# Optimization experiments

Measured on AMD Instinct MI355X. Metric: run time of the kernel, lower is better.

Reference implementation:

```python
import jax, jax.numpy as jnp
import numpy as np

B, S, H, NH = 2, 2048, 2048, 16
HD = H // NH  # head_dim = 128


def setup_inputs() -> dict:
    key = jax.random.key(0)
    ks = jax.random.split(key, 6)
    scale = 1.0 / np.sqrt(H)
    hidden_state = jax.random.normal(ks[0], (B, S, H), dtype=jnp.float32)
    # upper-triangular (strictly above diagonal) = 1 -> masked positions
    causal_mask = jnp.triu(jnp.ones((S, S), dtype=jnp.float32), k=1)[None, None]
    Wq = jax.random.normal(ks[1], (H, H), dtype=jnp.float32) * scale
    Wk = jax.random.normal(ks[2], (H, H), dtype=jnp.float32) * scale
    Wv = jax.random.normal(ks[3], (H, H), dtype=jnp.float32) * scale
    Wo = jax.random.normal(ks[4], (H, H), dtype=jnp.float32) * scale
    zeros = jnp.zeros((H,), dtype=jnp.float32)
    return {"hidden_state": hidden_state, "causal_mask": causal_mask,
            "Wq": Wq, "bq": zeros, "Wk": Wk, "bk": zeros,
            "Wv": Wv, "bv": zeros, "Wo": Wo, "bo": zeros}


def reference(hidden_state, causal_mask, Wq, bq, Wk, bk, Wv, bv, Wo, bo):
    b, s, h = hidden_state.shape
    q = (hidden_state @ Wq.T + bq).reshape(b, s, NH, HD).transpose(0, 2, 1, 3)  # [B,NH,S,HD]
    k = (hidden_state @ Wk.T + bk).reshape(b, s, NH, HD).transpose(0, 2, 1, 3)
    v = (hidden_state @ Wv.T + bv).reshape(b, s, NH, HD).transpose(0, 2, 1, 3)
    scores = jnp.einsum('bhqd,bhkd->bhqk', q, k) / jnp.sqrt(jnp.float32(HD))
    scores = scores + causal_mask * (-1e9)
    probs = jax.nn.softmax(scores, axis=-1)
    out = jnp.einsum('bhqk,bhkd->bhqd', probs, v)
    out = out.transpose(0, 2, 1, 3).reshape(b, s, h)
    return out @ Wo.T + bo
```

## Files before the change

kernel.cpp:

```cpp
#include <hip/hip_runtime.h>
#include <hip/hip_bf16.h>
#include <stdint.h>

#define B_   2
#define S_   2048
#define H_   2048
#define NH_  16
#define HD_  128
#define MTOT (B_*S_)

typedef __attribute__((ext_vector_type(8))) short bf16x8;
typedef __attribute__((ext_vector_type(4))) short bf16x4;
typedef __attribute__((ext_vector_type(4))) float f32x4;

__device__ __forceinline__ void gload_lds16(const void* g, void* l) {
    __builtin_amdgcn_global_load_lds(
        (const __attribute__((address_space(1))) void*)g,
        (__attribute__((address_space(3))) void*)l, 16, 0, 0);
}

__device__ __forceinline__ unsigned short f2bfu(float x) {
    __hip_bfloat16 h = __float2bfloat16(x);
    return *reinterpret_cast<unsigned short*>(&h);
}
__device__ __forceinline__ int packbf(float a, float b) {
    return (int)f2bfu(a) | ((int)f2bfu(b) << 16);
}

#define BAR()  asm volatile("s_barrier" ::: "memory")
#define WLG0() asm volatile("s_waitcnt lgkmcnt(0)" ::: "memory")
#define WVM(n) asm volatile("s_waitcnt vmcnt(" #n ")" ::: "memory")

__global__ void castall(const float* __restrict__ hs,
                        const float* __restrict__ w0, const float* __restrict__ w1,
                        const float* __restrict__ w2, const float* __restrict__ w3,
                        __hip_bfloat16* __restrict__ xb,
                        __hip_bfloat16* __restrict__ o0, __hip_bfloat16* __restrict__ o1,
                        __hip_bfloat16* __restrict__ o2, __hip_bfloat16* __restrict__ o3)
{
    const size_t Q = 1048576;
    const float* in; __hip_bfloat16* out; size_t base = 0;
    switch (blockIdx.y) {
        case 0:  in = hs; out = xb; break;
        case 1:  in = hs; out = xb; base = Q; break;
        case 2:  in = w0; out = o0; break;
        case 3:  in = w1; out = o1; break;
        case 4:  in = w2; out = o2; break;
        default: in = w3; out = o3; break;
    }
    size_t i = base + (size_t)blockIdx.x * 256 + threadIdx.x;
    float4 v = *(const float4*)(in + i * 4);
    uint2 o;
    o.x = (unsigned)packbf(v.x, v.y);
    o.y = (unsigned)packbf(v.z, v.w);
    *(uint2*)((char*)out + i * 8) = o;
}

template<int EPI>
__device__ __forceinline__ void gemm256x128_body(const __hip_bfloat16* __restrict__ Xp,
                                                 const __hip_bfloat16* __restrict__ Wp,
                                                 const float* __restrict__ bias,
                                                 void* __restrict__ Cout,
                                                 int bm, int bn, char* smem)
{
    const int tid  = threadIdx.x;
    const int wave = tid >> 6, lane = tid & 63;
    const int quad = lane >> 4, l16 = lane & 15;
    const int wr = wave >> 2, wc = wave & 3;

    const int ro = l16 * 64;
    const int co = (((l16 & 8) ? ((quad * 8) ^ 16) : (quad * 8)) << 1);

    int r0, c0, r1, c1;
    {
        int D = tid * 16;
        int rg = D >> 11, cg = (D >> 10) & 1;
        int rr = (D >> 6) & 15, c = (D & 63) >> 1;
        int cs = (rr & 8) ? (c ^ 16) : c;
        r0 = rg * 16 + rr;  c0 = cg * 32 + cs;
        D = 8192 + tid * 16;
        rg = D >> 11; cg = (D >> 10) & 1;
        rr = (D >> 6) & 15; c = (D & 63) >> 1;
        cs = (rr & 8) ? (c ^ 16) : c;
        r1 = rg * 16 + rr;  c1 = cg * 32 + cs;
    }

    char* const A0h = smem + wr * 16384;
    char* const A1h = smem + 32768 + wr * 16384;
    char* const B0h = smem + 65536 + (wc >> 1) * 8192;
    char* const B1h = smem + 81920 + (wc >> 1) * 8192;
    const int bsub = (wc & 1) * 2;

    auto STG = [&](char* ldsb, const __hip_bfloat16* g) {
        gload_lds16(g + (size_t)r0 * H_ + c0, ldsb + wave * 1024);
        gload_lds16(g + (size_t)r1 * H_ + c1, ldsb + 8192 + wave * 1024);
    };
    auto STG1 = [&](char* ldsb, const __hip_bfloat16* g) {
        gload_lds16(g + (size_t)r0 * H_ + c0, ldsb + wave * 1024);
    };
    auto SRCA = [&](const __hip_bfloat16* P, int t, int hf) {
        return P + (size_t)(hf * 128) * H_ + (size_t)t * 64;
    };
    auto SRCB = [&](const __hip_bfloat16* P, int t, int hf) {
        return P + (size_t)(hf * 64) * H_ + (size_t)t * 64;
    };

    f32x4 acc[8][2] = {};

    STG (smem,          SRCA(Xp, 0, 0));
    STG (smem + 16384,  SRCA(Xp, 0, 1));
    STG1(smem + 65536,        SRCB(Wp, 0, 0));
    STG1(smem + 65536 + 8192, SRCB(Wp, 0, 1));
    STG1(smem + 81920,        SRCB(Wp, 1, 0));
    STG1(smem + 81920 + 8192, SRCB(Wp, 1, 1));
    WVM(2);
    BAR();

    const int NIT = H_ / 128;
    bf16x8 bfr[2][2];
    for (int j = 0; j < NIT; ++j) {
        const bool more = (j < NIT - 1);
        const int t1 = 2 * j + 1;
#pragma unroll
        for (int ph = 0; ph < 8; ++ph) {
            const int p = ph & 3;
            char* aA = (ph < 4) ? A0h : A1h;
            char* aB = (ph < 4) ? B0h : B1h;

            if (p == 0) {
#pragma unroll
                for (int jj = 0; jj < 2; ++jj)
#pragma unroll
                    for (int kk = 0; kk < 2; ++kk)
                        bfr[jj][kk] = *(const bf16x8*)(aB + ((bsub + jj) * 2 + kk) * 1024 + ro + co);
            }
            bf16x8 af[2][2];
#pragma unroll
            for (int i2 = 0; i2 < 2; ++i2)
#pragma unroll
                for (int kk = 0; kk < 2; ++kk)
                    af[i2][kk] = *(const bf16x8*)(aA + ((2 * p + i2) * 2 + kk) * 1024 + ro + co);

            if (ph == 0) { STG(smem + 32768, SRCA(Xp, t1, 0));
                           STG(smem + 49152, SRCA(Xp, t1, 1)); }
            else if (ph == 1 && more) STG1(smem + 65536,        SRCB(Wp, t1 + 1, 0));
            else if (ph == 2 && more) STG1(smem + 65536 + 8192, SRCB(Wp, t1 + 1, 1));
            else if (ph == 4 && more) STG (smem,                SRCA(Xp, t1 + 1, 0));
            else if (ph == 5 && more) STG (smem + 16384,        SRCA(Xp, t1 + 1, 1));
            else if (ph == 6 && more) STG1(smem + 81920,        SRCB(Wp, t1 + 2, 0));
            else if (ph == 7 && more) STG1(smem + 81920 + 8192, SRCB(Wp, t1 + 2, 1));

            if (ph == 3) { if (more) { WVM(2); } else { WVM(0); } }
            if (ph == 7 && more) { WVM(2); }

            BAR();
            WLG0();
            __builtin_amdgcn_sched_barrier(0);
            __builtin_amdgcn_s_setprio(1);
#pragma unroll
            for (int kk = 0; kk < 2; ++kk)
#pragma unroll
                for (int i2 = 0; i2 < 2; ++i2)
#pragma unroll
                    for (int jj = 0; jj < 2; ++jj)
                        acc[2 * p + i2][jj] = __builtin_amdgcn_mfma_f32_16x16x32_bf16(
                            af[i2][kk], bfr[jj][kk], acc[2 * p + i2][jj], 0, 0, 0);
            __builtin_amdgcn_s_setprio(0);
            BAR();
        }
    }

    if (EPI == 2) {
        __hip_bfloat16* VTo = (__hip_bfloat16*)Cout;
#pragma unroll
        for (int i = 0; i < 8; ++i) {
            int tok = bm * 256 + wr * 128 + i * 16 + quad * 4;
            int b = tok >> 11, s = tok & (S_ - 1);
#pragma unroll
            for (int jj = 0; jj < 2; ++jj) {
                int col = bn * 128 + (wc >> 1) * 64 + (wc & 1) * 32 + jj * 16 + l16;
                int h = col >> 7, d = col & 127;
                float bv = bias[col];
                bf16x4 v;
#pragma unroll
                for (int r = 0; r < 4; ++r)
                    v[r] = (short)f2bfu(acc[i][jj][r] + bv);
                *(bf16x4*)(VTo + ((size_t)(b * 16 + h) * 128 + d) * S_ + s) = v;
            }
        }
    } else {
#pragma unroll
        for (int i = 0; i < 8; ++i) {
            int row = bm * 256 + wr * 128 + i * 16 + quad * 4;
#pragma unroll
            for (int jj = 0; jj < 2; ++jj) {
                int col = bn * 128 + (wc >> 1) * 64 + (wc & 1) * 32 + jj * 16 + l16;
                float bv = bias[col];
#pragma unroll
                for (int r = 0; r < 4; ++r) {
                    float v = acc[i][jj][r] + bv;
                    if (EPI == 1)
                        ((__hip_bfloat16*)Cout)[(size_t)(row + r) * H_ + col] = __float2bfloat16(v);
                    else
                        ((float*)Cout)[(size_t)(row + r) * H_ + col] = v;
                }
            }
        }
    }
}

__global__ __launch_bounds__(512, 2)
void gemm_qkv8(const __hip_bfloat16* __restrict__ X,
               const __hip_bfloat16* __restrict__ Wq, const __hip_bfloat16* __restrict__ Wk,
               const __hip_bfloat16* __restrict__ Wv,
               const float* __restrict__ bq, const float* __restrict__ bk,
               const float* __restrict__ bv,
               __hip_bfloat16* __restrict__ Qo, __hip_bfloat16* __restrict__ Ko,
               __hip_bfloat16* __restrict__ VTo)
{
    __shared__ __align__(16) char smem[98304];

    const int bid = blockIdx.x;
    const int swz = (bid & 7) * 96 + (bid >> 3);
    const int sel = swz >> 8;
    const int rem = swz & 255;
    const int bn  = rem & 15;
    const int bm  = rem >> 4;

    const __hip_bfloat16* W = (sel == 0) ? Wq : (sel == 1) ? Wk : Wv;
    const float* bias       = (sel == 0) ? bq : (sel == 1) ? bk : bv;

    const __hip_bfloat16* Xp = X + (size_t)(bm * 256) * H_;
    const __hip_bfloat16* Wp = W + (size_t)(bn * 128) * H_;

    if (sel == 2)
        gemm256x128_body<2>(Xp, Wp, bias, VTo, bm, bn, smem);
    else
        gemm256x128_body<1>(Xp, Wp, bias, (sel == 0) ? Qo : Ko, bm, bn, smem);
}

__global__ __launch_bounds__(512, 2)
void gemm_out8(const __hip_bfloat16* __restrict__ A, const __hip_bfloat16* __restrict__ W,
               const float* __restrict__ bias, float* __restrict__ C)
{
    __shared__ __align__(16) char smem[98304];
    const int bid = blockIdx.x;
    const int swz = (bid & 7) * 32 + (bid >> 3);
    const int bn  = swz & 15;
    const int bm  = swz >> 4;
    gemm256x128_body<0>(A + (size_t)(bm * 256) * H_, W + (size_t)(bn * 128) * H_,
                        bias, C, bm, bn, smem);
}

__global__ __launch_bounds__(256, 2)
void attn_kernel(const __hip_bfloat16* __restrict__ Q,
                 const __hip_bfloat16* __restrict__ K,
                 const __hip_bfloat16* __restrict__ VT,
                 __hip_bfloat16* __restrict__ O)
{
    __shared__ __align__(16) char Ks[2][16384];
    __shared__ __align__(16) char Vt[2][16384];

    const int tid  = threadIdx.x;
    const int wave = tid >> 6, lane = tid & 63;
    const int quad = lane >> 4, l16 = lane & 15;

    const int lid = blockIdx.x;
    const int xcd = lid & 7;
    const int q   = lid >> 3;
    const int grp = q >> 4;
    const int k15 = q & 15;
    const int bh  = (grp << 3) | xcd;
    const int u   = (grp < 2) ? (15 - k15) : k15;
    const int b   = bh >> 4, h = bh & 15;
    const int qbA = 2 * u, qbB = 2 * u + 1;

    const size_t headoff = (size_t)b * S_ * H_ + (size_t)h * HD_;
    const __hip_bfloat16* Qp  = Q + headoff;
    const __hip_bfloat16* Kp  = K + headoff;
    const __hip_bfloat16* Vtp = VT + (size_t)(b * 16 + h) * 128 * S_;

    const float scale  = 0.08838834764831843f;
    const float THRraw = 90.50966799187809f;
    const int A0 = (((quad & 1) * 2) * 16 + l16) * 4;
    const int A1 = A0 + 64;
    const bool hiq = (quad >= 2);

    const int qrow_local = wave * 16;
    const int qrowA = qbA * 64 + qrow_local;
    const int qrowB = qbB * 64 + qrow_local;

    bf16x8 qfA[4], qfB[4];
#pragma unroll
    for (int kd = 0; kd < 4; ++kd) {
        qfA[kd] = *(const bf16x8*)(Qp + (size_t)(qrowA + l16) * H_ + kd * 32 + quad * 8);
        qfB[kd] = *(const bf16x8*)(Qp + (size_t)(qrowB + l16) * H_ + kd * 32 + quad * 8);
    }

    f32x4 oaccA[8] = {}, oaccB[8] = {};
    float miA = -1e30f, liA = 0.0f;
    float miB = -1e30f, liB = 0.0f;

    auto sm_xform = [&](f32x4 (&sacc)[4], float& mi, float& li, f32x4 (&oacc)[8],
                        bool diag, bf16x8 (&pf)[2]) {
        float p[4][4];
        float tm = -1e30f;
#pragma unroll
        for (int cb = 0; cb < 4; ++cb)
#pragma unroll
            for (int r = 0; r < 4; ++r) {
                float s = sacc[cb][r];
                if (diag) {
                    int keyl = cb * 16 + quad * 4 + r;
                    if (keyl > qrow_local + l16) s = -1e30f;
                }
                p[cb][r] = s;
                tm = fmaxf(tm, s);
            }
        tm = fmaxf(tm, __shfl_xor(tm, 16));
        tm = fmaxf(tm, __shfl_xor(tm, 32));

        const bool noresc = __all(tm - mi <= THRraw);
        float mnew = noresc ? mi : fmaxf(mi, tm);
        float ms = mnew * scale;

        float sum = 0.0f;
#pragma unroll
        for (int cb = 0; cb < 4; ++cb)
#pragma unroll
            for (int r = 0; r < 4; ++r) {
                float e = __expf(__builtin_fmaf(p[cb][r], scale, -ms));
                p[cb][r] = e;
                sum += e;
            }
        sum += __shfl_xor(sum, 16);
        sum += __shfl_xor(sum, 32);

        if (noresc) {
            li = li + sum;
        } else {
            float alpha = __expf((mi - mnew) * scale);
            li = li * alpha + sum;
            float ar[4];
#pragma unroll
            for (int r = 0; r < 4; ++r)
                ar[r] = __shfl(alpha, quad * 4 + r);
#pragma unroll
            for (int db = 0; db < 8; ++db)
#pragma unroll
                for (int r = 0; r < 4; ++r)
                    oacc[db][r] *= ar[r];
        }
        mi = mnew;

        int Pp[4][2];
#pragma unroll
        for (int cb = 0; cb < 4; ++cb) {
            Pp[cb][0] = packbf(p[cb][0], p[cb][1]);
            Pp[cb][1] = packbf(p[cb][2], p[cb][3]);
        }
#pragma unroll
        for (int ks = 0; ks < 2; ++ks) {
            int c0 = 2 * ks, c1 = 2 * ks + 1;
            int d0 = __builtin_amdgcn_ds_bpermute(A0, Pp[c0][0]);
            int e0 = __builtin_amdgcn_ds_bpermute(A0, Pp[c1][0]);
            int d1 = __builtin_amdgcn_ds_bpermute(A0, Pp[c0][1]);
            int e1 = __builtin_amdgcn_ds_bpermute(A0, Pp[c1][1]);
            int d2 = __builtin_amdgcn_ds_bpermute(A1, Pp[c0][0]);
            int e2 = __builtin_amdgcn_ds_bpermute(A1, Pp[c1][0]);
            int d3 = __builtin_amdgcn_ds_bpermute(A1, Pp[c0][1]);
            int e3 = __builtin_amdgcn_ds_bpermute(A1, Pp[c1][1]);
            union { int i[4]; bf16x8 v; } w;
            w.i[0] = hiq ? e0 : d0;
            w.i[1] = hiq ? e1 : d1;
            w.i[2] = hiq ? e2 : d2;
            w.i[3] = hiq ? e3 : d3;
            pf[ks] = w.v;
        }
    };

#pragma unroll
    for (int t = 0; t < 4; ++t) {
        int c = wave * 256 + t * 64 + lane;
        int krow = c >> 4, kpos = c & 15;
        gload_lds16(Kp + (size_t)krow * H_ + (kpos ^ (krow & 7)) * 8,
                    &Ks[0][(wave * 256 + t * 64) * 16]);
        int vrow = c >> 3, vpos = c & 7;
        gload_lds16(Vtp + (size_t)vrow * S_ + (vpos ^ (vrow & 7)) * 8,
                    &Vt[0][(wave * 256 + t * 64) * 16]);
    }
    __syncthreads();

    for (int kb = 0; kb <= qbB; ++kb) {
        const int cur = kb & 1;
        const bool more   = (kb < qbB);
        const bool aliveA = (kb <= qbA);

        if (more) {
            const __hip_bfloat16* Kn = Kp + (size_t)(kb + 1) * 64 * H_;
            const int vcol = (kb + 1) * 64;
#pragma unroll
            for (int t = 0; t < 4; ++t) {
                int c = wave * 256 + t * 64 + lane;
                int krow = c >> 4, kpos = c & 15;
                gload_lds16(Kn + (size_t)krow * H_ + (kpos ^ (krow & 7)) * 8,
                            &Ks[cur ^ 1][(wave * 256 + t * 64) * 16]);
                int vrow = c >> 3, vpos = c & 7;
                gload_lds16(Vtp + (size_t)vrow * S_ + vcol + (vpos ^ (vrow & 7)) * 8,
                            &Vt[cur ^ 1][(wave * 256 + t * 64) * 16]);
            }
        }

        f32x4 saccA[4] = {}, saccB[4] = {};
#pragma unroll
        for (int cb = 0; cb < 4; ++cb) {
#pragma unroll
            for (int kd = 0; kd < 4; ++kd) {
                int row = cb * 16 + l16;
                int pos = (4 * kd + quad) ^ (l16 & 7);
                bf16x8 kf = *(const bf16x8*)&Ks[cur][row * 256 + pos * 16];
                saccA[cb] = __builtin_amdgcn_mfma_f32_16x16x32_bf16(kf, qfA[kd], saccA[cb], 0, 0, 0);
                saccB[cb] = __builtin_amdgcn_mfma_f32_16x16x32_bf16(kf, qfB[kd], saccB[cb], 0, 0, 0);
            }
        }

        bf16x8 pfA[2], pfB[2];
        if (aliveA) sm_xform(saccA, miA, liA, oaccA, kb == qbA, pfA);
        sm_xform(saccB, miB, liB, oaccB, kb == qbB, pfB);

        if (aliveA) {
#pragma unroll
            for (int ks = 0; ks < 2; ++ks)
#pragma unroll
                for (int db = 0; db < 8; ++db) {
                    int vrow = db * 16 + l16;
                    int vpos = (ks * 4 + quad) ^ (l16 & 7);
                    bf16x8 vf = *(const bf16x8*)&Vt[cur][vrow * 128 + vpos * 16];
                    oaccA[db] = __builtin_amdgcn_mfma_f32_16x16x32_bf16(pfA[ks], vf, oaccA[db], 0, 0, 0);
                    oaccB[db] = __builtin_amdgcn_mfma_f32_16x16x32_bf16(pfB[ks], vf, oaccB[db], 0, 0, 0);
                }
        } else {
#pragma unroll
            for (int ks = 0; ks < 2; ++ks)
#pragma unroll
                for (int db = 0; db < 8; ++db) {
                    int vrow = db * 16 + l16;
                    int vpos = (ks * 4 + quad) ^ (l16 & 7);
                    bf16x8 vf = *(const bf16x8*)&Vt[cur][vrow * 128 + vpos * 16];
                    oaccB[db] = __builtin_amdgcn_mfma_f32_16x16x32_bf16(pfB[ks], vf, oaccB[db], 0, 0, 0);
                }
        }

        __syncthreads();
    }

    {
        float lr[4];
#pragma unroll
        for (int r = 0; r < 4; ++r)
            lr[r] = __shfl(liA, quad * 4 + r);
#pragma unroll
        for (int db = 0; db < 8; ++db)
#pragma unroll
            for (int r = 0; r < 4; ++r) {
                float v = oaccA[db][r] / lr[r];
                size_t row = (size_t)b * S_ + qrowA + quad * 4 + r;
                O[row * H_ + h * HD_ + db * 16 + l16] = __float2bfloat16(v);
            }
    }
    {
        float lr[4];
#pragma unroll
        for (int r = 0; r < 4; ++r)
            lr[r] = __shfl(liB, quad * 4 + r);
#pragma unroll
        for (int db = 0; db < 8; ++db)
#pragma unroll
            for (int r = 0; r < 4; ++r) {
                float v = oaccB[db][r] / lr[r];
                size_t row = (size_t)b * S_ + qrowB + quad * 4 + r;
                O[row * H_ + h * HD_ + db * 16 + l16] = __float2bfloat16(v);
            }
    }
}

extern "C" void kernel_launch(void* const* d_in, const int* in_sizes, int n_in,
                              void* d_out, int out_size, void* d_ws, size_t ws_size,
                              hipStream_t stream)
{
    const float* hs = (const float*)d_in[0];
    const float* Wq = (const float*)d_in[2];
    const float* bq = (const float*)d_in[3];
    const float* Wk = (const float*)d_in[4];
    const float* bk = (const float*)d_in[5];
    const float* Wv = (const float*)d_in[6];
    const float* bv = (const float*)d_in[7];
    const float* Wo = (const float*)d_in[8];
    const float* bo = (const float*)d_in[9];

    const size_t szX = (size_t)MTOT * H_;
    const size_t szW = (size_t)H_ * H_;

    __hip_bfloat16* Xbf = (__hip_bfloat16*)d_ws;
    __hip_bfloat16* Wqb = Xbf + szX;
    __hip_bfloat16* Wkb = Wqb + szW;
    __hip_bfloat16* Wvb = Wkb + szW;
    __hip_bfloat16* Wob = Wvb + szW;
    __hip_bfloat16* Qb  = Wob + szW;
    __hip_bfloat16* Kb  = Qb + szX;
    __hip_bfloat16* VTb = Kb + szX;

    castall<<<dim3(4096, 6), 256, 0, stream>>>(hs, Wq, Wk, Wv, Wo, Xbf, Wqb, Wkb, Wvb, Wob);

    gemm_qkv8<<<dim3(768), 512, 0, stream>>>(Xbf, Wqb, Wkb, Wvb, bq, bk, bv, Qb, Kb, VTb);

    attn_kernel<<<dim3(512), 256, 0, stream>>>(Qb, Kb, VTb, Xbf);

    gemm_out8<<<dim3(256), 512, 0, stream>>>(Xbf, Wob, bo, (float*)d_out);
}
```

Baseline: 371.6 us.

## Fuse Q and K projections into one block sharing the X tile

Adds a QK body in which each block computes both the Q and K output tiles for the same X rows. The X tile is loaded once from LDS and fed to two sets of MFMAs. This cuts X global loads and the block count for the QKV projection from 768 to 512 blocks, with 256 of them doing double work. In exchange the kernel needs 128KB of LDS and twice the accumulator registers, which can lower occupancy below the two-blocks-per-CU launch bound and unbalance Q/K blocks against V blocks.

```diff
diff --git a/kernel.cpp b/kernel.cpp
--- a/kernel.cpp
+++ b/kernel.cpp
@@ -56,23 +56,17 @@
     *(uint2*)((char*)out + i * 8) = o;
 }
 
-template<int EPI>
-__device__ __forceinline__ void gemm256x128_body(const __hip_bfloat16* __restrict__ Xp,
-                                                 const __hip_bfloat16* __restrict__ Wp,
-                                                 const float* __restrict__ bias,
-                                                 void* __restrict__ Cout,
-                                                 int bm, int bn, char* smem)
-{
-    const int tid  = threadIdx.x;
-    const int wave = tid >> 6, lane = tid & 63;
-    const int quad = lane >> 4, l16 = lane & 15;
-    const int wr = wave >> 2, wc = wave & 3;
-
-    const int ro = l16 * 64;
-    const int co = (((l16 & 8) ? ((quad * 8) ^ 16) : (quad * 8)) << 1);
-
+struct TileIdx {
+    int tid, wave, lane, quad, l16, wr, wc, ro, co, bsub;
     int r0, c0, r1, c1;
-    {
+    __device__ __forceinline__ TileIdx() {
+        tid = threadIdx.x;
+        wave = tid >> 6; lane = tid & 63;
+        quad = lane >> 4; l16 = lane & 15;
+        wr = wave >> 2; wc = wave & 3;
+        ro = l16 * 64;
+        co = (((l16 & 8) ? ((quad * 8) ^ 16) : (quad * 8)) << 1);
+        bsub = (wc & 1) * 2;
         int D = tid * 16;
         int rg = D >> 11, cg = (D >> 10) & 1;
         int rr = (D >> 6) & 15, c = (D & 63) >> 1;
@@ -84,19 +78,28 @@
         cs = (rr & 8) ? (c ^ 16) : c;
         r1 = rg * 16 + rr;  c1 = cg * 32 + cs;
     }
-
-    char* const A0h = smem + wr * 16384;
-    char* const A1h = smem + 32768 + wr * 16384;
-    char* const B0h = smem + 65536 + (wc >> 1) * 8192;
-    char* const B1h = smem + 81920 + (wc >> 1) * 8192;
-    const int bsub = (wc & 1) * 2;
+};
+
+template<int EPI>
+__device__ __forceinline__ void gemm256x128_body(const __hip_bfloat16* __restrict__ Xp,
+                                                 const __hip_bfloat16* __restrict__ Wp,
+                                                 const float* __restrict__ bias,
+                                                 void* __restrict__ Cout,
+                                                 int bm, int bn, char* smem)
+{
+    TileIdx ix;
+
+    char* const A0h = smem + ix.wr * 16384;
+    char* const A1h = smem + 32768 + ix.wr * 16384;
+    char* const B0h = smem + 65536 + (ix.wc >> 1) * 8192;
+    char* const B1h = smem + 81920 + (ix.wc >> 1) * 8192;
 
     auto STG = [&](char* ldsb, const __hip_bfloat16* g) {
-        gload_lds16(g + (size_t)r0 * H_ + c0, ldsb + wave * 1024);
-        gload_lds16(g + (size_t)r1 * H_ + c1, ldsb + 8192 + wave * 1024);
+        gload_lds16(g + (size_t)ix.r0 * H_ + ix.c0, ldsb + ix.wave * 1024);
+        gload_lds16(g + (size_t)ix.r1 * H_ + ix.c1, ldsb + 8192 + ix.wave * 1024);
     };
     auto STG1 = [&](char* ldsb, const __hip_bfloat16* g) {
-        gload_lds16(g + (size_t)r0 * H_ + c0, ldsb + wave * 1024);
+        gload_lds16(g + (size_t)ix.r0 * H_ + ix.c0, ldsb + ix.wave * 1024);
     };
     auto SRCA = [&](const __hip_bfloat16* P, int t, int hf) {
         return P + (size_t)(hf * 128) * H_ + (size_t)t * 64;
@@ -132,14 +135,14 @@
                 for (int jj = 0; jj < 2; ++jj)
 #pragma unroll
                     for (int kk = 0; kk < 2; ++kk)
-                        bfr[jj][kk] = *(const bf16x8*)(aB + ((bsub + jj) * 2 + kk) * 1024 + ro + co);
+                        bfr[jj][kk] = *(const bf16x8*)(aB + ((ix.bsub + jj) * 2 + kk) * 1024 + ix.ro + ix.co);
             }
             bf16x8 af[2][2];
 #pragma unroll
             for (int i2 = 0; i2 < 2; ++i2)
 #pragma unroll
                 for (int kk = 0; kk < 2; ++kk)
-                    af[i2][kk] = *(const bf16x8*)(aA + ((2 * p + i2) * 2 + kk) * 1024 + ro + co);
+                    af[i2][kk] = *(const bf16x8*)(aA + ((2 * p + i2) * 2 + kk) * 1024 + ix.ro + ix.co);
 
             if (ph == 0) { STG(smem + 32768, SRCA(Xp, t1, 0));
                            STG(smem + 49152, SRCA(Xp, t1, 1)); }
@@ -174,11 +177,11 @@
         __hip_bfloat16* VTo = (__hip_bfloat16*)Cout;
 #pragma unroll
         for (int i = 0; i < 8; ++i) {
-            int tok = bm * 256 + wr * 128 + i * 16 + quad * 4;
+            int tok = bm * 256 + ix.wr * 128 + i * 16 + ix.quad * 4;
             int b = tok >> 11, s = tok & (S_ - 1);
 #pragma unroll
             for (int jj = 0; jj < 2; ++jj) {
-                int col = bn * 128 + (wc >> 1) * 64 + (wc & 1) * 32 + jj * 16 + l16;
+                int col = bn * 128 + (ix.wc >> 1) * 64 + (ix.wc & 1) * 32 + jj * 16 + ix.l16;
                 int h = col >> 7, d = col & 127;
                 float bv = bias[col];
                 bf16x4 v;
@@ -191,26 +194,148 @@
     } else {
 #pragma unroll
         for (int i = 0; i < 8; ++i) {
-            int row = bm * 256 + wr * 128 + i * 16 + quad * 4;
+            int row = bm * 256 + ix.wr * 128 + i * 16 + ix.quad * 4;
 #pragma unroll
             for (int jj = 0; jj < 2; ++jj) {
-                int col = bn * 128 + (wc >> 1) * 64 + (wc & 1) * 32 + jj * 16 + l16;
+                int col = bn * 128 + (ix.wc >> 1) * 64 + (ix.wc & 1) * 32 + jj * 16 + ix.l16;
                 float bv = bias[col];
 #pragma unroll
-                for (int r = 0; r < 4; ++r) {
-                    float v = acc[i][jj][r] + bv;
-                    if (EPI == 1)
-                        ((__hip_bfloat16*)Cout)[(size_t)(row + r) * H_ + col] = __float2bfloat16(v);
-                    else
-                        ((float*)Cout)[(size_t)(row + r) * H_ + col] = v;
-                }
+                for (int r = 0; r < 4; ++r)
+                    ((float*)Cout)[(size_t)(row + r) * H_ + col] = acc[i][jj][r] + bv;
+            }
+        }
+    }
+}
+
+__device__ __forceinline__ void gemm256x128_qk_body(const __hip_bfloat16* __restrict__ Xp,
+                                                    const __hip_bfloat16* __restrict__ Wqp,
+                                                    const __hip_bfloat16* __restrict__ Wkp,
+                                                    const float* __restrict__ bq,
+                                                    const float* __restrict__ bk,
+                                                    __hip_bfloat16* __restrict__ Qo,
+                                                    __hip_bfloat16* __restrict__ Ko,
+                                                    int bm, int bn, char* smem)
+{
+    TileIdx ix;
+
+    char* const A0h  = smem + ix.wr * 16384;
+    char* const A1h  = smem + 32768 + ix.wr * 16384;
+    char* const Bq0h = smem + 65536  + (ix.wc >> 1) * 8192;
+    char* const Bq1h = smem + 81920  + (ix.wc >> 1) * 8192;
+    char* const Bk0h = smem + 98304  + (ix.wc >> 1) * 8192;
+    char* const Bk1h = smem + 114688 + (ix.wc >> 1) * 8192;
+
+    auto STG = [&](char* ldsb, const __hip_bfloat16* g) {
+        gload_lds16(g + (size_t)ix.r0 * H_ + ix.c0, ldsb + ix.wave * 1024);
+        gload_lds16(g + (size_t)ix.r1 * H_ + ix.c1, ldsb + 8192 + ix.wave * 1024);
+    };
+    auto STG1 = [&](char* ldsb, const __hip_bfloat16* g) {
+        gload_lds16(g + (size_t)ix.r0 * H_ + ix.c0, ldsb + ix.wave * 1024);
+    };
+    auto SRCA = [&](const __hip_bfloat16* P, int t, int hf) {
+        return P + (size_t)(hf * 128) * H_ + (size_t)t * 64;
+    };
+    auto SRCB = [&](const __hip_bfloat16* P, int t, int hf) {
+        return P + (size_t)(hf * 64) * H_ + (size_t)t * 64;
+    };
+
+    f32x4 accq[8][2] = {}, acck[8][2] = {};
+
+    STG (smem,                  SRCA(Xp, 0, 0));
+    STG (smem + 16384,          SRCA(Xp, 0, 1));
+    STG1(smem + 65536,          SRCB(Wqp, 0, 0));
+    STG1(smem + 65536 + 8192,   SRCB(Wqp, 0, 1));
+    STG1(smem + 98304,          SRCB(Wkp, 0, 0));
+    STG1(smem + 98304 + 8192,   SRCB(Wkp, 0, 1));
+    STG1(smem + 81920,          SRCB(Wqp, 1, 0));
+    STG1(smem + 81920 + 8192,   SRCB(Wqp, 1, 1));
+    STG1(smem + 114688,         SRCB(Wkp, 1, 0));
+    STG1(smem + 114688 + 8192,  SRCB(Wkp, 1, 1));
+    WVM(4);
+    BAR();
+
+    const int NIT = H_ / 128;
+    bf16x8 bfq[2][2], bfk[2][2];
+    for (int j = 0; j < NIT; ++j) {
+        const bool more = (j < NIT - 1);
+        const int t1 = 2 * j + 1;
+#pragma unroll
+        for (int ph = 0; ph < 8; ++ph) {
+            const int p = ph & 3;
+            char* aA  = (ph < 4) ? A0h  : A1h;
+            char* aBq = (ph < 4) ? Bq0h : Bq1h;
+            char* aBk = (ph < 4) ? Bk0h : Bk1h;
+
+            if (p == 0) {
+#pragma unroll
+                for (int jj = 0; jj < 2; ++jj)
+#pragma unroll
+                    for (int kk = 0; kk < 2; ++kk) {
+                        bfq[jj][kk] = *(const bf16x8*)(aBq + ((ix.bsub + jj) * 2 + kk) * 1024 + ix.ro + ix.co);
+                        bfk[jj][kk] = *(const bf16x8*)(aBk + ((ix.bsub + jj) * 2 + kk) * 1024 + ix.ro + ix.co);
+                    }
+            }
+            bf16x8 af[2][2];
+#pragma unroll
+            for (int i2 = 0; i2 < 2; ++i2)
+#pragma unroll
+                for (int kk = 0; kk < 2; ++kk)
+                    af[i2][kk] = *(const bf16x8*)(aA + ((2 * p + i2) * 2 + kk) * 1024 + ix.ro + ix.co);
+
+            if (ph == 0) { STG(smem + 32768, SRCA(Xp, t1, 0));
+                           STG(smem + 49152, SRCA(Xp, t1, 1)); }
+            else if (ph == 1 && more) { STG1(smem + 65536,         SRCB(Wqp, t1 + 1, 0));
+                                        STG1(smem + 65536 + 8192,  SRCB(Wqp, t1 + 1, 1)); }
+            else if (ph == 2 && more) { STG1(smem + 98304,         SRCB(Wkp, t1 + 1, 0));
+                                        STG1(smem + 98304 + 8192,  SRCB(Wkp, t1 + 1, 1)); }
+            else if (ph == 4 && more) STG(smem,          SRCA(Xp, t1 + 1, 0));
+            else if (ph == 5 && more) STG(smem + 16384,  SRCA(Xp, t1 + 1, 1));
+            else if (ph == 6 && more) { STG1(smem + 81920,         SRCB(Wqp, t1 + 2, 0));
+                                        STG1(smem + 81920 + 8192,  SRCB(Wqp, t1 + 2, 1)); }
+            else if (ph == 7 && more) { STG1(smem + 114688,        SRCB(Wkp, t1 + 2, 0));
+                                        STG1(smem + 114688 + 8192, SRCB(Wkp, t1 + 2, 1)); }
+
+            if (ph == 3) { if (more) { WVM(4); } else { WVM(0); } }
+            if (ph == 7 && more) { WVM(4); }
+
+            BAR();
+            WLG0();
+            __builtin_amdgcn_sched_barrier(0);
+            __builtin_amdgcn_s_setprio(1);
+#pragma unroll
+            for (int kk = 0; kk < 2; ++kk)
+#pragma unroll
+                for (int i2 = 0; i2 < 2; ++i2)
+#pragma unroll
+                    for (int jj = 0; jj < 2; ++jj) {
+                        accq[2 * p + i2][jj] = __builtin_amdgcn_mfma_f32_16x16x32_bf16(
+                            af[i2][kk], bfq[jj][kk], accq[2 * p + i2][jj], 0, 0, 0);
+                        acck[2 * p + i2][jj] = __builtin_amdgcn_mfma_f32_16x16x32_bf16(
+                            af[i2][kk], bfk[jj][kk], acck[2 * p + i2][jj], 0, 0, 0);
+                    }
+            __builtin_amdgcn_s_setprio(0);
+            BAR();
+        }
+    }
+
+#pragma unroll
+    for (int i = 0; i < 8; ++i) {
+        int row = bm * 256 + ix.wr * 128 + i * 16 + ix.quad * 4;
+#pragma unroll
+        for (int jj = 0; jj < 2; ++jj) {
+            int col = bn * 128 + (ix.wc >> 1) * 64 + (ix.wc & 1) * 32 + jj * 16 + ix.l16;
+            float bvq = bq[col], bvk = bk[col];
+#pragma unroll
+            for (int r = 0; r < 4; ++r) {
+                Qo[(size_t)(row + r) * H_ + col] = __float2bfloat16(accq[i][jj][r] + bvq);
+                Ko[(size_t)(row + r) * H_ + col] = __float2bfloat16(acck[i][jj][r] + bvk);
             }
         }
     }
 }
 
 __global__ __launch_bounds__(512, 2)
-void gemm_qkv8(const __hip_bfloat16* __restrict__ X,
+void gemm_qkvf(const __hip_bfloat16* __restrict__ X,
                const __hip_bfloat16* __restrict__ Wq, const __hip_bfloat16* __restrict__ Wk,
                const __hip_bfloat16* __restrict__ Wv,
                const float* __restrict__ bq, const float* __restrict__ bk,
@@ -218,25 +343,24 @@
                __hip_bfloat16* __restrict__ Qo, __hip_bfloat16* __restrict__ Ko,
                __hip_bfloat16* __restrict__ VTo)
 {
-    __shared__ __align__(16) char smem[98304];
+    __shared__ __align__(16) char smem[131072];
 
     const int bid = blockIdx.x;
-    const int swz = (bid & 7) * 96 + (bid >> 3);
-    const int sel = swz >> 8;
-    const int rem = swz & 255;
-    const int bn  = rem & 15;
-    const int bm  = rem >> 4;
-
-    const __hip_bfloat16* W = (sel == 0) ? Wq : (sel == 1) ? Wk : Wv;
-    const float* bias       = (sel == 0) ? bq : (sel == 1) ? bk : bv;
-
-    const __hip_bfloat16* Xp = X + (size_t)(bm * 256) * H_;
-    const __hip_bfloat16* Wp = W + (size_t)(bn * 128) * H_;
-
-    if (sel == 2)
-        gemm256x128_body<2>(Xp, Wp, bias, VTo, bm, bn, smem);
-    else
-        gemm256x128_body<1>(Xp, Wp, bias, (sel == 0) ? Qo : Ko, bm, bn, smem);
+    if (bid < 256) {
+        const int swz = (bid & 7) * 32 + (bid >> 3);
+        const int bn  = swz & 15;
+        const int bm  = swz >> 4;
+        gemm256x128_qk_body(X + (size_t)(bm * 256) * H_,
+                            Wq + (size_t)(bn * 128) * H_, Wk + (size_t)(bn * 128) * H_,
+                            bq, bk, Qo, Ko, bm, bn, smem);
+    } else {
+        const int b2  = bid - 256;
+        const int swz = (b2 & 7) * 32 + (b2 >> 3);
+        const int bn  = swz & 15;
+        const int bm  = swz >> 4;
+        gemm256x128_body<2>(X + (size_t)(bm * 256) * H_, Wv + (size_t)(bn * 128) * H_,
+                            bv, VTo, bm, bn, smem);
+    }
 }
 
 __global__ __launch_bounds__(512, 2)
@@ -512,7 +636,7 @@
 
     castall<<<dim3(4096, 6), 256, 0, stream>>>(hs, Wq, Wk, Wv, Wo, Xbf, Wqb, Wkb, Wvb, Wob);
 
-    gemm_qkv8<<<dim3(768), 512, 0, stream>>>(Xbf, Wqb, Wkb, Wvb, bq, bk, bv, Qb, Kb, VTb);
+    gemm_qkvf<<<dim3(512), 512, 0, stream>>>(Xbf, Wqb, Wkb, Wvb, bq, bk, bv, Qb, Kb, VTb);
 
     attn_kernel<<<dim3(512), 256, 0, stream>>>(Qb, Kb, VTb, Xbf);
 
```

Result: faster. 360.5 us (-3.0%).
